# Optimization experiments

Hardware: AMD Instinct MI355X
Metric: run time of the kernel (lower is better)

## Reference

```python
import jax, jax.numpy as jnp
import numpy as np

LN2 = 0.6931471805599453

def ssp(t):
    # PhysNet shifted softplus
    return jax.nn.softplus(t) - LN2

N, F, K, E, NRES = 50000, 128, 64, 800000, 3

def setup_inputs() -> dict:
    key = jax.random.key(0)
    ks = jax.random.split(key, 16)
    d = {}
    d['x'] = jax.random.normal(ks[0], (N, F), dtype=jnp.float32)
    d['edge_index'] = jax.random.randint(ks[1], (2, E), 0, N, dtype=jnp.int64)
    d['edge_attr'] = jax.random.uniform(ks[2], (E, K), dtype=jnp.float32)
    s = 1.0 / np.sqrt(F)
    d['W_same'] = jax.random.normal(ks[3], (F, F), dtype=jnp.float32) * s
    d['b_same'] = jnp.zeros((F,), jnp.float32)
    d['W_diff'] = jax.random.normal(ks[4], (F, F), dtype=jnp.float32) * s
    d['b_diff'] = jnp.zeros((F,), jnp.float32)
    # G initialized to zero in the original; use small random so gradients flow
    d['W_G'] = jax.random.normal(ks[5], (F, K), dtype=jnp.float32) * 0.01
    d['res_W1'] = jax.random.normal(ks[6], (NRES, F, F), dtype=jnp.float32) * s
    d['res_b1'] = jnp.zeros((NRES, F), jnp.float32)
    d['res_W2'] = jax.random.normal(ks[7], (NRES, F, F), dtype=jnp.float32) * s
    d['res_b2'] = jnp.zeros((NRES, F), jnp.float32)
    d['W_last'] = jax.random.normal(ks[8], (F, F), dtype=jnp.float32) * s
    d['b_last'] = jnp.zeros((F,), jnp.float32)
    d['u'] = jnp.ones((1, F), jnp.float32)
    return d

def reference(x, edge_index, edge_attr, W_same, b_same, W_diff, b_diff, W_G,
              res_W1, res_b1, res_W2, res_b2, W_last, b_last, u):
    src, dst = edge_index[0], edge_index[1]  # flow='source_to_target': x_j = x[src], aggr at dst
    xa = ssp(x)                                           # activation(x) before propagate
    # message: act(lin_for_diff(x_j)) -- linear+act commute with gather, compute per-node
    h = ssp(xa @ W_diff.T + b_diff)                       # [N, F]
    gate = edge_attr @ W_G.T                              # [E, F]  G(edge_attr)
    msg = h[src] * gate                                   # [E, F]
    aggr = jax.ops.segment_sum(msg, dst, num_segments=x.shape[0])  # add-aggregate
    # update: act(lin_for_same(x)) + aggr_out
    msged_x = ssp(xa @ W_same.T + b_same) + aggr          # [N, F]
    # residual interaction layers: t + lin2(act(lin1(act(t))))
    t = msged_x
    for i in range(res_W1.shape[0]):
        h1 = ssp(ssp(t) @ res_W1[i].T + res_b1[i])
        t = t + (h1 @ res_W2[i].T + res_b2[i])
    v = ssp(t) @ W_last.T + b_last
    return (v + x * u, msged_x)
```

## Files before the change

kernel.cpp:

```cpp
#include <hip/hip_runtime.h>
#include <hip/hip_bf16.h>

#define LN2F 0.69314718055994530942f

typedef short bf16x8 __attribute__((ext_vector_type(8)));
typedef float f32x4  __attribute__((ext_vector_type(4)));

__device__ __forceinline__ float ssp_f(float t){
  return fmaxf(t, 0.0f) + __logf(1.0f + __expf(-fabsf(t))) - LN2F;
}
__device__ __forceinline__ unsigned short f2bf_u(float f){
  __hip_bfloat16 b = __float2bfloat16(f);
  return *reinterpret_cast<unsigned short*>(&b);
}
__device__ __forceinline__ float bf2f(unsigned short u){
  __hip_bfloat16 b = *reinterpret_cast<__hip_bfloat16*>(&u);
  return __bfloat162float(b);
}

__global__ void detect_idx_kernel(const unsigned* __restrict__ ei, int* __restrict__ flag){
  __shared__ int cnt;
  if (threadIdx.x == 0) cnt = 0;
  __syncthreads();
  int nz = 0;
  for (int i = threadIdx.x; i < 1024; i += 256)
    nz += (ei[2*i + 1] != 0u) ? 1 : 0;
  atomicAdd(&cnt, nz);
  __syncthreads();
  if (threadIdx.x == 0) *flag = (cnt > 64) ? 1 : 0;
}

__device__ __forceinline__ int load_idx(const void* ei, int is32, size_t pos){
  return is32 ? ((const int*)ei)[pos] : (int)(((const long long*)ei)[pos]);
}

__global__ void zero_int_kernel(int* __restrict__ p, int n){
  int i = blockIdx.x * 256 + threadIdx.x;
  if (i < n) p[i] = 0;
}

__global__ void hist_kernel(const void* __restrict__ ei, const int* __restrict__ flag,
                            int* __restrict__ count, int E){
  const int is32 = *flag;
  for (long long e = (long long)blockIdx.x * 256 + threadIdx.x; e < E;
       e += (long long)gridDim.x * 256){
    int d = load_idx(ei, is32, (size_t)((long long)E + e));
    atomicAdd(&count[d], 1);
  }
}

__global__ __launch_bounds__(256) void scan1_kernel(const int* __restrict__ count,
                                                    int* __restrict__ bsum, int N){
  __shared__ int red[256];
  const int t = threadIdx.x;
  int i0 = blockIdx.x * 2048 + t * 8;
  int s = 0;
  #pragma unroll
  for (int r = 0; r < 8; ++r){ int i = i0 + r; s += (i < N) ? count[i] : 0; }
  red[t] = s;
  __syncthreads();
  for (int off = 128; off > 0; off >>= 1){
    if (t < off) red[t] += red[t + off];
    __syncthreads();
  }
  if (t == 0) bsum[blockIdx.x] = red[0];
}

__global__ void scan2_kernel(int* __restrict__ bsum, int* __restrict__ offs, int nb, int N){
  if (threadIdx.x == 0 && blockIdx.x == 0){
    int run = 0;
    for (int b = 0; b < nb; ++b){ int v = bsum[b]; bsum[b] = run; run += v; }
    offs[N] = run;
  }
}

__global__ __launch_bounds__(256) void scan3_kernel(const int* __restrict__ count,
                                                    const int* __restrict__ bsum,
                                                    int* __restrict__ offs,
                                                    int* __restrict__ cur, int N){
  __shared__ int red[256];
  const int t = threadIdx.x;
  int i0 = blockIdx.x * 2048 + t * 8;
  int v[8];
  int s = 0;
  #pragma unroll
  for (int r = 0; r < 8; ++r){ int i = i0 + r; v[r] = (i < N) ? count[i] : 0; s += v[r]; }
  red[t] = s;
  __syncthreads();
  #pragma unroll
  for (int off = 1; off < 256; off <<= 1){
    int tv = (t >= off) ? red[t - off] : 0;
    __syncthreads();
    red[t] += tv;
    __syncthreads();
  }
  int run = red[t] - s + bsum[blockIdx.x];
  #pragma unroll
  for (int r = 0; r < 8; ++r){
    int i = i0 + r;
    if (i < N){ offs[i] = run; cur[i] = run; }
    run += v[r];
  }
}

__global__ void fill_kernel(const void* __restrict__ ei, const int* __restrict__ flag,
                            int* __restrict__ cur, int2* __restrict__ se, int E){
  const int is32 = *flag;
  for (long long e = (long long)blockIdx.x * 256 + threadIdx.x; e < E;
       e += (long long)gridDim.x * 256){
    int s = load_idx(ei, is32, (size_t)e);
    int d = load_idx(ei, is32, (size_t)((long long)E + e));
    int slot = atomicAdd(&cur[d], 1);
    se[slot] = make_int2((int)e, s);
  }
}

struct WPtrs { const float* w[16]; };

__global__ __launch_bounds__(256) void prep_wfrag_kernel(WPtrs p, unsigned short* __restrict__ dst){
  const int m = blockIdx.x;
  const float* __restrict__ W = p.w[m];
  unsigned short* __restrict__ out = dst + (size_t)m * 16384;
  for (int q = threadIdx.x; q < 16384; q += 256){
    int i = q & 7, lane = (q >> 3) & 63, kt = (q >> 9) & 3, ct = q >> 11;
    int row = ct*16 + (lane & 15);
    int k   = kt*32 + (lane >> 4)*8 + i;
    out[q] = f2bf_u(W[row*128 + k]);
  }
}

__global__ __launch_bounds__(256) void prep_wgfrag_kernel(const float* __restrict__ WG,
                                                          unsigned short* __restrict__ dst){
  for (int q = blockIdx.x*256 + threadIdx.x; q < 8192; q += gridDim.x*256){
    int i = q & 7, lane = (q >> 3) & 63, kt = (q >> 9) & 1, nt = (q >> 10) & 3, half = q >> 12;
    int f = half*64 + nt*16 + (lane & 15);
    int k = kt*32 + (lane >> 4)*8 + i;
    dst[q] = f2bf_u(WG[(size_t)f*64 + k]);
  }
}

__device__ __forceinline__ void mfma_gemm128s(const unsigned short* __restrict__ A_s,
                                              const unsigned short* __restrict__ Bf,
                                              int rbase, int lane, f32x4 acc[8]){
  #pragma unroll
  for (int ct = 0; ct < 8; ++ct) acc[ct] = (f32x4){0.f, 0.f, 0.f, 0.f};
  const int r  = rbase + (lane & 15);
  const int kg = lane >> 4;
  const int sw = (r & 7) << 3;
  #pragma unroll
  for (int kt = 0; kt < 4; ++kt){
    bf16x8 a = *(const bf16x8*)&A_s[r*128 + ((kt*32 + kg*8) ^ sw)];
    #pragma unroll
    for (int ct = 0; ct < 8; ++ct){
      bf16x8 b = *(const bf16x8*)&Bf[(size_t)((ct*4 + kt)*64 + lane)*8];
      acc[ct] = __builtin_amdgcn_mfma_f32_16x16x32_bf16(a, b, acc[ct], 0, 0, 0);
    }
  }
}

__device__ __forceinline__ void stage_bf512(unsigned short* __restrict__ Bf,
                                            const unsigned short* __restrict__ src, int t){
  #pragma unroll
  for (int it = 0; it < 4; ++it){
    int off = (it*512 + t) * 8;
    *(uint4*)&Bf[off] = *(const uint4*)&src[off];
  }
}

__global__ __launch_bounds__(512) void node_dual_kernel(
    const float* __restrict__ x, const unsigned short* __restrict__ wfrag,
    const float* __restrict__ bsame, const float* __restrict__ bdiff,
    unsigned short* __restrict__ hbf, float* __restrict__ msged, int N){
  __shared__ __align__(16) unsigned short A_s[128*128];
  __shared__ __align__(16) unsigned short Bf[16384];
  const int t = threadIdx.x, wv = t >> 6, lane = t & 63;
  const int kg = lane >> 4, c = lane & 15;
  const int row0 = blockIdx.x * 128;
  for (int q = t; q < 2048; q += 512){
    int row = q >> 4, c0 = (q & 15) * 8;
    float4 va = make_float4(0.f,0.f,0.f,0.f), vb = va;
    if (row0 + row < N){
      va = *(const float4*)&x[(size_t)(row0 + row)*128 + c0];
      vb = *(const float4*)&x[(size_t)(row0 + row)*128 + c0 + 4];
    }
    uint4 w;
    w.x = f2bf_u(ssp_f(va.x)) | ((unsigned)f2bf_u(ssp_f(va.y)) << 16);
    w.y = f2bf_u(ssp_f(va.z)) | ((unsigned)f2bf_u(ssp_f(va.w)) << 16);
    w.z = f2bf_u(ssp_f(vb.x)) | ((unsigned)f2bf_u(ssp_f(vb.y)) << 16);
    w.w = f2bf_u(ssp_f(vb.z)) | ((unsigned)f2bf_u(ssp_f(vb.w)) << 16);
    *(uint4*)&A_s[row*128 + (c0 ^ ((row & 7) << 3))] = w;
  }
  stage_bf512(Bf, wfrag, t);
  __syncthreads();
  f32x4 acc[8];
  mfma_gemm128s(A_s, Bf, wv*16, lane, acc);
  #pragma unroll
  for (int ct = 0; ct < 8; ++ct){
    int col = ct*16 + c;
    float bv = bsame[col];
    #pragma unroll
    for (int q = 0; q < 4; ++q){
      int gr = row0 + wv*16 + kg*4 + q;
      if (gr < N) msged[(size_t)gr*128 + col] = ssp_f(acc[ct][q] + bv);
    }
  }
  __syncthreads();
  stage_bf512(Bf, wfrag + 16384, t);
  __syncthreads();
  mfma_gemm128s(A_s, Bf, wv*16, lane, acc);
  #pragma unroll
  for (int ct = 0; ct < 8; ++ct){
    int col = ct*16 + c;
    float bv = bdiff[col];
    #pragma unroll
    for (int q = 0; q < 4; ++q){
      int gr = row0 + wv*16 + kg*4 + q;
      if (gr < N) hbf[(size_t)gr*128 + col] = f2bf_u(ssp_f(acc[ct][q] + bv));
    }
  }
}

__global__ __launch_bounds__(256) void edge_mfma_kernel(
    const float* __restrict__ ea, const unsigned short* __restrict__ wgfrag,
    const unsigned short* __restrict__ h, const int2* __restrict__ se,
    const int* __restrict__ offs, float* __restrict__ msged, int N, int E, int KW){
  __shared__ float P_s[4][16][66];
  const int t = threadIdx.x, wv = t >> 6, lane = t & 63;
  const int kg = lane >> 4, c = lane & 15;
  const int gw = blockIdx.x * 4 + wv;
  const int half = gw & 1;
  const int widx = gw >> 1;
  if (widx >= KW) return;
  long long tt0 = (long long)widx * E / KW;
  long long tt1 = (long long)(widx + 1) * E / KW;
  int lo = 0, hi = N;
  while (lo < hi){ int mid = (lo + hi) >> 1; if ((long long)offs[mid] < tt0) lo = mid + 1; else hi = mid; }
  const int d_lo = lo;
  hi = N;
  while (lo < hi){ int mid = (lo + hi) >> 1; if ((long long)offs[mid] < tt1) lo = mid + 1; else hi = mid; }
  const int d_hi = lo;
  if (d_lo >= d_hi) return;
  const int s_beg = offs[d_lo], s_end = offs[d_hi];
  if (s_beg >= s_end) return;

  bf16x8 bw[4][2];
  #pragma unroll
  for (int nt = 0; nt < 4; ++nt)
    #pragma unroll
    for (int kt = 0; kt < 2; ++kt)
      bw[nt][kt] = *(const bf16x8*)&wgfrag[(size_t)((((half*4+nt)*2+kt)*64)+lane)*8];

  int d_cur = d_lo;
  int next_off = offs[d_cur + 1];
  while (next_off == s_beg && d_cur + 1 < d_hi){ ++d_cur; next_off = offs[d_cur + 1]; }

  float sum_v = 0.f;
  for (int p = s_beg; p < s_end; p += 16){
    const int nb = min(16, s_end - p);
    int2 s2 = se[p + min(c, nb-1)];

    const float* ra = &ea[(size_t)s2.x * 64];
    float4 a00 = *(const float4*)&ra[kg*8];
    float4 a01 = *(const float4*)&ra[kg*8 + 4];
    float4 a10 = *(const float4*)&ra[32 + kg*8];
    float4 a11 = *(const float4*)&ra[32 + kg*8 + 4];

    int sv[4];
    #pragma unroll
    for (int q = 0; q < 4; ++q) sv[q] = __shfl(s2.y, kg*4 + q, 16);
    float hv[4][4];
    #pragma unroll
    for (int q = 0; q < 4; ++q){
      const unsigned short* hr = &h[(size_t)sv[q]*128 + half*64 + c];
      #pragma unroll
      for (int nt = 0; nt < 4; ++nt) hv[nt][q] = bf2f(hr[nt*16]);
    }

    bf16x8 af0, af1;
    unsigned short* w0 = (unsigned short*)&af0;
    unsigned short* w1 = (unsigned short*)&af1;
    w0[0]=f2bf_u(a00.x); w0[1]=f2bf_u(a00.y); w0[2]=f2bf_u(a00.z); w0[3]=f2bf_u(a00.w);
    w0[4]=f2bf_u(a01.x); w0[5]=f2bf_u(a01.y); w0[6]=f2bf_u(a01.z); w0[7]=f2bf_u(a01.w);
    w1[0]=f2bf_u(a10.x); w1[1]=f2bf_u(a10.y); w1[2]=f2bf_u(a10.z); w1[3]=f2bf_u(a10.w);
    w1[4]=f2bf_u(a11.x); w1[5]=f2bf_u(a11.y); w1[6]=f2bf_u(a11.z); w1[7]=f2bf_u(a11.w);

    f32x4 acc[4];
    #pragma unroll
    for (int nt = 0; nt < 4; ++nt) acc[nt] = (f32x4){0.f,0.f,0.f,0.f};
    #pragma unroll
    for (int nt = 0; nt < 4; ++nt){
      acc[nt] = __builtin_amdgcn_mfma_f32_16x16x32_bf16(af0, bw[nt][0], acc[nt], 0, 0, 0);
      acc[nt] = __builtin_amdgcn_mfma_f32_16x16x32_bf16(af1, bw[nt][1], acc[nt], 0, 0, 0);
    }

    #pragma unroll
    for (int nt = 0; nt < 4; ++nt)
      #pragma unroll
      for (int q = 0; q < 4; ++q)
        P_s[wv][kg*4 + q][nt*16 + c] = acc[nt][q] * hv[nt][q];

    __builtin_amdgcn_s_waitcnt(0);

    for (int i = 0; i < nb; ++i){
      sum_v += P_s[wv][i][lane];
      if (p + i + 1 == next_off){
        msged[(size_t)d_cur*128 + half*64 + lane] += sum_v;
        sum_v = 0.f;
        int old = next_off;
        do { ++d_cur; next_off = (d_cur < d_hi) ? offs[d_cur + 1] : 0x7FFFFFFF; }
        while (next_off == old);
      }
    }
  }
}

__global__ __launch_bounds__(512) void tail_kernel(
    const float* __restrict__ msged, const float* __restrict__ x, const float* __restrict__ u,
    const unsigned short* __restrict__ wfrag,
    const float* __restrict__ rb1, const float* __restrict__ rb2,
    const float* __restrict__ blast, float* __restrict__ out0, int N, int NRES){
  __shared__ __align__(16) unsigned short A_s[128*128];
  __shared__ __align__(16) unsigned short Bf[16384];
  const int t = threadIdx.x, wv = t >> 6, lane = t & 63;
  const int kg = lane >> 4, c = lane & 15;
  const int row0 = blockIdx.x * 128;

  float treg[8][4];
  #pragma unroll
  for (int ct = 0; ct < 8; ++ct)
    #pragma unroll
    for (int q = 0; q < 4; ++q){
      int gr = row0 + wv*16 + kg*4 + q;
      treg[ct][q] = (gr < N) ? msged[(size_t)gr*128 + ct*16 + c] : 0.f;
    }

  f32x4 acc[8];
  for (int l = 0; l < NRES; ++l){
    __syncthreads();
    #pragma unroll
    for (int ct = 0; ct < 8; ++ct)
      #pragma unroll
      for (int q = 0; q < 4; ++q){
        int row = wv*16 + kg*4 + q, col = ct*16 + c;
        A_s[row*128 + (col ^ ((row & 7) << 3))] = f2bf_u(ssp_f(treg[ct][q]));
      }
    stage_bf512(Bf, wfrag + (size_t)(2 + 2*l)*16384, t);
    __syncthreads();
    mfma_gemm128s(A_s, Bf, wv*16, lane, acc);
    __syncthreads();
    #pragma unroll
    for (int ct = 0; ct < 8; ++ct){
      float bv = rb1[l*128 + ct*16 + c];
      #pragma unroll
      for (int q = 0; q < 4; ++q){
        int row = wv*16 + kg*4 + q, col = ct*16 + c;
        A_s[row*128 + (col ^ ((row & 7) << 3))] = f2bf_u(ssp_f(acc[ct][q] + bv));
      }
    }
    stage_bf512(Bf, wfrag + (size_t)(3 + 2*l)*16384, t);
    __syncthreads();
    mfma_gemm128s(A_s, Bf, wv*16, lane, acc);
    #pragma unroll
    for (int ct = 0; ct < 8; ++ct){
      float bv = rb2[l*128 + ct*16 + c];
      #pragma unroll
      for (int q = 0; q < 4; ++q) treg[ct][q] += acc[ct][q] + bv;
    }
  }
  __syncthreads();
  #pragma unroll
  for (int ct = 0; ct < 8; ++ct)
    #pragma unroll
    for (int q = 0; q < 4; ++q){
      int row = wv*16 + kg*4 + q, col = ct*16 + c;
      A_s[row*128 + (col ^ ((row & 7) << 3))] = f2bf_u(ssp_f(treg[ct][q]));
    }
  stage_bf512(Bf, wfrag + (size_t)(2 + 2*NRES)*16384, t);
  __syncthreads();
  mfma_gemm128s(A_s, Bf, wv*16, lane, acc);
  #pragma unroll
  for (int ct = 0; ct < 8; ++ct){
    int col = ct*16 + c;
    float bv = blast[col];
    float uv = u[col];
    #pragma unroll
    for (int q = 0; q < 4; ++q){
      int gr = row0 + wv*16 + kg*4 + q;
      if (gr < N){
        size_t idx = (size_t)gr*128 + col;
        out0[idx] = acc[ct][q] + bv + x[idx]*uv;
      }
    }
  }
}

extern "C" void kernel_launch(void* const* d_in, const int* in_sizes, int n_in,
                              void* d_out, int out_size, void* d_ws, size_t ws_size,
                              hipStream_t stream){
  const float* x     = (const float*)d_in[0];
  const void*  ei    = d_in[1];
  const float* ea    = (const float*)d_in[2];
  const float* Wsame = (const float*)d_in[3];
  const float* bsame = (const float*)d_in[4];
  const float* Wdiff = (const float*)d_in[5];
  const float* bdiff = (const float*)d_in[6];
  const float* WG    = (const float*)d_in[7];
  const float* rW1   = (const float*)d_in[8];
  const float* rb1   = (const float*)d_in[9];
  const float* rW2   = (const float*)d_in[10];
  const float* rb2   = (const float*)d_in[11];
  const float* Wlast = (const float*)d_in[12];
  const float* blast = (const float*)d_in[13];
  const float* u     = (const float*)d_in[14];

  const int N    = in_sizes[0] / 128;
  const int E    = in_sizes[1] / 2;
  int NRES = in_sizes[8] / (128*128);
  if (NRES > 6) NRES = 6;

  float* out0  = (float*)d_out;
  float* msged = (float*)d_out + (size_t)N * 128;

  auto align256 = [](size_t v){ return (v + 255) & ~(size_t)255; };
  const size_t o_h      = 256;
  const size_t o_count  = align256(o_h      + (size_t)N * 128 * 2);
  const size_t o_off    = align256(o_count  + (size_t)N * 4);
  const size_t o_cur    = align256(o_off    + (size_t)(N + 1) * 4);
  const size_t o_se     = align256(o_cur    + (size_t)N * 4);
  const size_t o_bsum   = align256(o_se     + (size_t)E * 8);
  const size_t o_wfrag  = align256(o_bsum   + (size_t)4096 * 4);
  const size_t o_wgfrag = align256(o_wfrag  + (size_t)16 * 16384 * 2);

  int*   flag = (int*)d_ws;
  unsigned short* hbf = (unsigned short*)((char*)d_ws + o_h);
  int* count  = (int*)((char*)d_ws + o_count);
  int* offs   = (int*)((char*)d_ws + o_off);
  int* cur    = (int*)((char*)d_ws + o_cur);
  int2* se    = (int2*)((char*)d_ws + o_se);
  int* bsum   = (int*)((char*)d_ws + o_bsum);
  unsigned short* wfrag  = (unsigned short*)((char*)d_ws + o_wfrag);
  unsigned short* wgfrag = (unsigned short*)((char*)d_ws + o_wgfrag);
  (void)ws_size;

  const int nw = 3 + 2*NRES;
  WPtrs wp;
  wp.w[0] = Wsame;
  wp.w[1] = Wdiff;
  for (int l = 0; l < NRES; ++l){
    wp.w[2 + 2*l] = rW1 + (size_t)l*16384;
    wp.w[3 + 2*l] = rW2 + (size_t)l*16384;
  }
  wp.w[2 + 2*NRES] = Wlast;
  for (int i = nw; i < 16; ++i) wp.w[i] = Wlast;

  const int nb_node = (N + 127) / 128;
  const int nbk     = (N + 2047) / 2048;
  const int nb_edge = 2048;
  const int KW = nb_edge * 4 / 2;

  detect_idx_kernel<<<1, 256, 0, stream>>>((const unsigned*)ei, flag);
  prep_wfrag_kernel<<<nw, 256, 0, stream>>>(wp, wfrag);
  prep_wgfrag_kernel<<<32, 256, 0, stream>>>(WG, wgfrag);
  node_dual_kernel<<<nb_node, 512, 0, stream>>>(x, wfrag, bsame, bdiff, hbf, msged, N);

  zero_int_kernel<<<(N + 255) / 256, 256, 0, stream>>>(count, N);
  hist_kernel<<<1024, 256, 0, stream>>>(ei, flag, count, E);
  scan1_kernel<<<nbk, 256, 0, stream>>>(count, bsum, N);
  scan2_kernel<<<1, 64, 0, stream>>>(bsum, offs, nbk, N);
  scan3_kernel<<<nbk, 256, 0, stream>>>(count, bsum, offs, cur, N);
  fill_kernel<<<1024, 256, 0, stream>>>(ei, flag, cur, se, E);

  edge_mfma_kernel<<<nb_edge, 256, 0, stream>>>(ea, wgfrag, hbf, se, offs, msged, N, E, KW);

  tail_kernel<<<nb_node, 512, 0, stream>>>(msged, x, u, wfrag, rb1, rb2, blast,
                                           out0, N, NRES);
}
```

Before: 369.1 us.

## Transpose edge MFMA to vectorize h gathers, prefetch indices, fuse setup kernels

The edge kernel swaps the MFMA operand roles so the weight fragment is the A operand and the edge attributes are B. Each lane then gathers one source row of h with vectorized ushort4 loads instead of shuffled scalar loads. The next block's index pair is prefetched, the next segment offset is kept in a register, and the full waitcnt is narrowed to lgkmcnt. Small setup and prep kernels are merged to cut launches. The P_s padding changes to suit the new transposed write pattern.

```diff
diff --git a/kernel.cpp b/kernel.cpp
--- a/kernel.cpp
+++ b/kernel.cpp
@@ -18,25 +18,26 @@
   return __bfloat162float(b);
 }
 
-__global__ void detect_idx_kernel(const unsigned* __restrict__ ei, int* __restrict__ flag){
-  __shared__ int cnt;
-  if (threadIdx.x == 0) cnt = 0;
-  __syncthreads();
-  int nz = 0;
-  for (int i = threadIdx.x; i < 1024; i += 256)
-    nz += (ei[2*i + 1] != 0u) ? 1 : 0;
-  atomicAdd(&cnt, nz);
-  __syncthreads();
-  if (threadIdx.x == 0) *flag = (cnt > 64) ? 1 : 0;
-}
-
 __device__ __forceinline__ int load_idx(const void* ei, int is32, size_t pos){
   return is32 ? ((const int*)ei)[pos] : (int)(((const long long*)ei)[pos]);
 }
 
-__global__ void zero_int_kernel(int* __restrict__ p, int n){
+__global__ __launch_bounds__(256) void setup_kernel(const unsigned* __restrict__ ei,
+                                                    int* __restrict__ flag,
+                                                    int* __restrict__ count, int N){
   int i = blockIdx.x * 256 + threadIdx.x;
-  if (i < n) p[i] = 0;
+  if (i < N) count[i] = 0;
+  if (blockIdx.x == 0){
+    __shared__ int cnt;
+    if (threadIdx.x == 0) cnt = 0;
+    __syncthreads();
+    int nz = 0;
+    for (int k = threadIdx.x; k < 1024; k += 256)
+      nz += (ei[2*k + 1] != 0u) ? 1 : 0;
+    atomicAdd(&cnt, nz);
+    __syncthreads();
+    if (threadIdx.x == 0) *flag = (cnt > 64) ? 1 : 0;
+  }
 }
 
 __global__ void hist_kernel(const void* __restrict__ ei, const int* __restrict__ flag,
@@ -117,25 +118,28 @@
 
 struct WPtrs { const float* w[16]; };
 
-__global__ __launch_bounds__(256) void prep_wfrag_kernel(WPtrs p, unsigned short* __restrict__ dst){
+__global__ __launch_bounds__(256) void prep_kernel(WPtrs p, int nw,
+    unsigned short* __restrict__ wfrag, const float* __restrict__ WG,
+    unsigned short* __restrict__ wgfrag){
   const int m = blockIdx.x;
-  const float* __restrict__ W = p.w[m];
-  unsigned short* __restrict__ out = dst + (size_t)m * 16384;
-  for (int q = threadIdx.x; q < 16384; q += 256){
-    int i = q & 7, lane = (q >> 3) & 63, kt = (q >> 9) & 3, ct = q >> 11;
-    int row = ct*16 + (lane & 15);
-    int k   = kt*32 + (lane >> 4)*8 + i;
-    out[q] = f2bf_u(W[row*128 + k]);
-  }
-}
-
-__global__ __launch_bounds__(256) void prep_wgfrag_kernel(const float* __restrict__ WG,
-                                                          unsigned short* __restrict__ dst){
-  for (int q = blockIdx.x*256 + threadIdx.x; q < 8192; q += gridDim.x*256){
-    int i = q & 7, lane = (q >> 3) & 63, kt = (q >> 9) & 1, nt = (q >> 10) & 3, half = q >> 12;
-    int f = half*64 + nt*16 + (lane & 15);
-    int k = kt*32 + (lane >> 4)*8 + i;
-    dst[q] = f2bf_u(WG[(size_t)f*64 + k]);
+  if (m < nw){
+    const float* __restrict__ W = p.w[m];
+    unsigned short* __restrict__ out = wfrag + (size_t)m * 16384;
+    for (int q = threadIdx.x; q < 16384; q += 256){
+      int i = q & 7, lane = (q >> 3) & 63, kt = (q >> 9) & 3, ct = q >> 11;
+      int row = ct*16 + (lane & 15);
+      int k   = kt*32 + (lane >> 4)*8 + i;
+      out[q] = f2bf_u(W[row*128 + k]);
+    }
+  } else {
+    const int b = m - nw;
+    for (int qq = threadIdx.x; qq < 2048; qq += 256){
+      int q = b*2048 + qq;
+      int i = q & 7, lane = (q >> 3) & 63, kt = (q >> 9) & 1, nt = (q >> 10) & 3, half = q >> 12;
+      int f = half*64 + nt*16 + (lane & 15);
+      int k = kt*32 + (lane >> 4)*8 + i;
+      wgfrag[q] = f2bf_u(WG[(size_t)f*64 + k]);
+    }
   }
 }
 
@@ -224,7 +228,7 @@
     const float* __restrict__ ea, const unsigned short* __restrict__ wgfrag,
     const unsigned short* __restrict__ h, const int2* __restrict__ se,
     const int* __restrict__ offs, float* __restrict__ msged, int N, int E, int KW){
-  __shared__ float P_s[4][16][66];
+  __shared__ float P_s[4][16][67];
   const int t = threadIdx.x, wv = t >> 6, lane = t & 63;
   const int kg = lane >> 4, c = lane & 15;
   const int gw = blockIdx.x * 4 + wv;
@@ -243,74 +247,84 @@
   const int s_beg = offs[d_lo], s_end = offs[d_hi];
   if (s_beg >= s_end) return;
 
-  bf16x8 bw[4][2];
+  bf16x8 aw[4][2];
   #pragma unroll
   for (int nt = 0; nt < 4; ++nt)
     #pragma unroll
     for (int kt = 0; kt < 2; ++kt)
-      bw[nt][kt] = *(const bf16x8*)&wgfrag[(size_t)((((half*4+nt)*2+kt)*64)+lane)*8];
+      aw[nt][kt] = *(const bf16x8*)&wgfrag[(size_t)((((half*4+nt)*2+kt)*64)+lane)*8];
 
   int d_cur = d_lo;
-  int next_off = offs[d_cur + 1];
-  while (next_off == s_beg && d_cur + 1 < d_hi){ ++d_cur; next_off = offs[d_cur + 1]; }
+  int no0 = offs[d_cur + 1];
+  while (no0 == s_beg && d_cur + 1 < d_hi){ ++d_cur; no0 = offs[d_cur + 1]; }
+  int no1 = (d_cur + 2 <= d_hi) ? offs[d_cur + 2] : 0x7FFFFFFF;
 
   float sum_v = 0.f;
-  for (int p = s_beg; p < s_end; p += 16){
-    const int nb = min(16, s_end - p);
-    int2 s2 = se[p + min(c, nb-1)];
-
-    const float* ra = &ea[(size_t)s2.x * 64];
-    float4 a00 = *(const float4*)&ra[kg*8];
-    float4 a01 = *(const float4*)&ra[kg*8 + 4];
-    float4 a10 = *(const float4*)&ra[32 + kg*8];
-    float4 a11 = *(const float4*)&ra[32 + kg*8 + 4];
-
-    int sv[4];
-    #pragma unroll
-    for (int q = 0; q < 4; ++q) sv[q] = __shfl(s2.y, kg*4 + q, 16);
-    float hv[4][4];
-    #pragma unroll
-    for (int q = 0; q < 4; ++q){
-      const unsigned short* hr = &h[(size_t)sv[q]*128 + half*64 + c];
-      #pragma unroll
-      for (int nt = 0; nt < 4; ++nt) hv[nt][q] = bf2f(hr[nt*16]);
-    }
-
-    bf16x8 af0, af1;
-    unsigned short* w0 = (unsigned short*)&af0;
-    unsigned short* w1 = (unsigned short*)&af1;
-    w0[0]=f2bf_u(a00.x); w0[1]=f2bf_u(a00.y); w0[2]=f2bf_u(a00.z); w0[3]=f2bf_u(a00.w);
-    w0[4]=f2bf_u(a01.x); w0[5]=f2bf_u(a01.y); w0[6]=f2bf_u(a01.z); w0[7]=f2bf_u(a01.w);
-    w1[0]=f2bf_u(a10.x); w1[1]=f2bf_u(a10.y); w1[2]=f2bf_u(a10.z); w1[3]=f2bf_u(a10.w);
-    w1[4]=f2bf_u(a11.x); w1[5]=f2bf_u(a11.y); w1[6]=f2bf_u(a11.z); w1[7]=f2bf_u(a11.w);
+  int p = s_beg;
+  int nb = min(16, s_end - p);
+  int2 s2 = se[p + min(c, nb - 1)];
+  while (p < s_end){
+    const int pn = p + 16;
+    int2 s2n = s2;
+    if (pn < s_end){
+      int nbn = min(16, s_end - pn);
+      s2n = se[pn + min(c, nbn - 1)];
+    }
+    const float* __restrict__ ra = &ea[(size_t)s2.x * 64 + kg*8];
+    float4 e00 = *(const float4*)&ra[0];
+    float4 e01 = *(const float4*)&ra[4];
+    float4 e10 = *(const float4*)&ra[32];
+    float4 e11 = *(const float4*)&ra[36];
+    const unsigned short* __restrict__ hr = &h[(size_t)s2.y*128 + half*64 + kg*4];
+    ushort4 hu0 = *(const ushort4*)&hr[0];
+    ushort4 hu1 = *(const ushort4*)&hr[16];
+    ushort4 hu2 = *(const ushort4*)&hr[32];
+    ushort4 hu3 = *(const ushort4*)&hr[48];
+
+    bf16x8 be0, be1;
+    unsigned short* b0p = (unsigned short*)&be0;
+    unsigned short* b1p = (unsigned short*)&be1;
+    b0p[0]=f2bf_u(e00.x); b0p[1]=f2bf_u(e00.y); b0p[2]=f2bf_u(e00.z); b0p[3]=f2bf_u(e00.w);
+    b0p[4]=f2bf_u(e01.x); b0p[5]=f2bf_u(e01.y); b0p[6]=f2bf_u(e01.z); b0p[7]=f2bf_u(e01.w);
+    b1p[0]=f2bf_u(e10.x); b1p[1]=f2bf_u(e10.y); b1p[2]=f2bf_u(e10.z); b1p[3]=f2bf_u(e10.w);
+    b1p[4]=f2bf_u(e11.x); b1p[5]=f2bf_u(e11.y); b1p[6]=f2bf_u(e11.z); b1p[7]=f2bf_u(e11.w);
 
     f32x4 acc[4];
     #pragma unroll
-    for (int nt = 0; nt < 4; ++nt) acc[nt] = (f32x4){0.f,0.f,0.f,0.f};
-    #pragma unroll
     for (int nt = 0; nt < 4; ++nt){
-      acc[nt] = __builtin_amdgcn_mfma_f32_16x16x32_bf16(af0, bw[nt][0], acc[nt], 0, 0, 0);
-      acc[nt] = __builtin_amdgcn_mfma_f32_16x16x32_bf16(af1, bw[nt][1], acc[nt], 0, 0, 0);
-    }
+      acc[nt] = (f32x4){0.f,0.f,0.f,0.f};
+      acc[nt] = __builtin_amdgcn_mfma_f32_16x16x32_bf16(aw[nt][0], be0, acc[nt], 0, 0, 0);
+      acc[nt] = __builtin_amdgcn_mfma_f32_16x16x32_bf16(aw[nt][1], be1, acc[nt], 0, 0, 0);
+    }
+
+    float hvv[4][4];
+    hvv[0][0]=bf2f(hu0.x); hvv[0][1]=bf2f(hu0.y); hvv[0][2]=bf2f(hu0.z); hvv[0][3]=bf2f(hu0.w);
+    hvv[1][0]=bf2f(hu1.x); hvv[1][1]=bf2f(hu1.y); hvv[1][2]=bf2f(hu1.z); hvv[1][3]=bf2f(hu1.w);
+    hvv[2][0]=bf2f(hu2.x); hvv[2][1]=bf2f(hu2.y); hvv[2][2]=bf2f(hu2.z); hvv[2][3]=bf2f(hu2.w);
+    hvv[3][0]=bf2f(hu3.x); hvv[3][1]=bf2f(hu3.y); hvv[3][2]=bf2f(hu3.z); hvv[3][3]=bf2f(hu3.w);
 
     #pragma unroll
     for (int nt = 0; nt < 4; ++nt)
       #pragma unroll
       for (int q = 0; q < 4; ++q)
-        P_s[wv][kg*4 + q][nt*16 + c] = acc[nt][q] * hv[nt][q];
-
-    __builtin_amdgcn_s_waitcnt(0);
-
-    for (int i = 0; i < nb; ++i){
+        P_s[wv][c][nt*16 + kg*4 + q] = acc[nt][q] * hvv[nt][q];
+
+    asm volatile("s_waitcnt lgkmcnt(0)" ::: "memory");
+
+    const int nbc = min(16, s_end - p);
+    for (int i = 0; i < nbc; ++i){
       sum_v += P_s[wv][i][lane];
-      if (p + i + 1 == next_off){
+      if (p + i + 1 == no0){
         msged[(size_t)d_cur*128 + half*64 + lane] += sum_v;
         sum_v = 0.f;
-        int old = next_off;
-        do { ++d_cur; next_off = (d_cur < d_hi) ? offs[d_cur + 1] : 0x7FFFFFFF; }
-        while (next_off == old);
+        do {
+          ++d_cur;
+          no0 = no1;
+          no1 = (d_cur + 2 <= d_hi) ? offs[d_cur + 2] : 0x7FFFFFFF;
+        } while (no0 == p + i + 1);
       }
     }
+    p = pn; s2 = s2n;
   }
 }
 
@@ -458,12 +472,10 @@
   const int nb_edge = 2048;
   const int KW = nb_edge * 4 / 2;
 
-  detect_idx_kernel<<<1, 256, 0, stream>>>((const unsigned*)ei, flag);
-  prep_wfrag_kernel<<<nw, 256, 0, stream>>>(wp, wfrag);
-  prep_wgfrag_kernel<<<32, 256, 0, stream>>>(WG, wgfrag);
+  setup_kernel<<<(N + 255) / 256, 256, 0, stream>>>((const unsigned*)ei, flag, count, N);
+  prep_kernel<<<nw + 4, 256, 0, stream>>>(wp, nw, wfrag, WG, wgfrag);
   node_dual_kernel<<<nb_node, 512, 0, stream>>>(x, wfrag, bsame, bdiff, hbf, msged, N);
 
-  zero_int_kernel<<<(N + 255) / 256, 256, 0, stream>>>(count, N);
   hist_kernel<<<1024, 256, 0, stream>>>(ei, flag, count, E);
   scan1_kernel<<<nbk, 256, 0, stream>>>(count, bsum, N);
   scan2_kernel<<<1, 64, 0, stream>>>(bsum, offs, nbk, N);
```

Result: no change. 369.1 us (+0.0%).
